# Kernel optimization log

Measured on AMD Instinct MI355X. Metric: run time of the kernel, lower is better.

Reference implementation:

```python
import jax, jax.numpy as jnp
import numpy as np

B, M, C = 32, 64, 36
INPUT_DIM, HIDDEN, N_CLASS = 1024, 512, 1000
NEG_INF = -1e10


def setup_inputs() -> dict:
    key = jax.random.key(0)
    ks = jax.random.split(key, 16)
    s = 0.02
    return {
        "mention_embeddings": jax.random.normal(ks[0], (B, M, INPUT_DIM), jnp.float32),
        "class_labels": jax.random.uniform(ks[1], (B, C, N_CLASS), jnp.float32),
        "mention_mask": jnp.ones((B, M), jnp.float32),
        "class_mask": jnp.ones((B, C), jnp.float32),
        # visual_embedder: Linear(n_class, H) -> ReLU -> Linear(H, H)
        "vw1": jax.random.normal(ks[2], (N_CLASS, HIDDEN), jnp.float32) * s,
        "vb1": jnp.zeros((HIDDEN,), jnp.float32),
        "vw2": jax.random.normal(ks[3], (HIDDEN, HIDDEN), jnp.float32) * s,
        "vb2": jnp.zeros((HIDDEN,), jnp.float32),
        # mention_embedder: Linear(input_dim, H) -> ReLU -> Linear(H, H)
        "mw1": jax.random.normal(ks[4], (INPUT_DIM, HIDDEN), jnp.float32) * s,
        "mb1": jnp.zeros((HIDDEN,), jnp.float32),
        "mw2": jax.random.normal(ks[5], (HIDDEN, HIDDEN), jnp.float32) * s,
        "mb2": jnp.zeros((HIDDEN,), jnp.float32),
        # attention: Linear(H, H) -> ReLU -> Linear(H, 1)
        "aw1": jax.random.normal(ks[6], (HIDDEN, HIDDEN), jnp.float32) * s,
        "ab1": jnp.zeros((HIDDEN,), jnp.float32),
        "aw2": jax.random.normal(ks[7], (HIDDEN, 1), jnp.float32) * s,
        "ab2": jnp.zeros((1,), jnp.float32),
    }


def reference(mention_embeddings, class_labels, mention_mask, class_mask,
              vw1, vb1, vw2, vb2, mw1, mb1, mw2, mb2, aw1, ab1, aw2, ab2):
    # visual embeddings: (B, C, H)
    vis = jax.nn.relu(class_labels @ vw1 + vb1) @ vw2 + vb2
    # mention embeddings: (B, M, H)
    men = jax.nn.relu(mention_embeddings @ mw1 + mb1) @ mw2 + mb2
    # broadcast outer product: (B, M, C, H)
    prod = men[:, :, None, :] * vis[:, None, :, :]
    # 2-layer MLP attention score -> (B, M, C)
    h = jax.nn.relu(prod @ aw1 + ab1)
    attn = (h @ aw2 + ab2)[..., 0]
    # masking
    attn = attn * mention_mask[:, :, None] * class_mask[:, None, :]
    attn = jnp.where(attn != 0, attn, NEG_INF)
    return attn
```

## Files before the change

### kernel.cpp

```cpp
#include <hip/hip_runtime.h>

typedef _Float16 f16;
typedef _Float16 f16x8 __attribute__((ext_vector_type(8)));
typedef _Float16 f16x4 __attribute__((ext_vector_type(4)));
typedef float f32x4 __attribute__((ext_vector_type(4)));
typedef float fl4 __attribute__((ext_vector_type(4)));

#define NEG_INF_F (-1e10f)

__device__ __forceinline__ void stage16(const f16* g, f16* l) {
    __builtin_amdgcn_global_load_lds((const __attribute__((address_space(1))) void*)g,
                                     (__attribute__((address_space(3))) void*)l, 16, 0, 0);
}

__global__ __launch_bounds__(256) void prep2(const float* __restrict__ me,
                                             const float* __restrict__ mw1,
                                             const float* __restrict__ vw1,
                                             const float* __restrict__ mw2,
                                             const float* __restrict__ vw2,
                                             const float* __restrict__ aw1,
                                             const float* __restrict__ cl,
                                             f16* __restrict__ me_h,
                                             f16* __restrict__ mw1t, f16* __restrict__ vw1t,
                                             f16* __restrict__ mw2t, f16* __restrict__ vw2t,
                                             f16* __restrict__ aw1t, f16* __restrict__ cl_h) {
    int bx = blockIdx.x, t = threadIdx.x;
    if (bx < 1792) {
        __shared__ float tile[32][33];
        const float* src; f16* dst; int Ksrc, Kp, tid;
        if (bx < 512)       { src = mw1; dst = mw1t; Ksrc = 1024; Kp = 1024; tid = bx; }
        else if (bx < 1024) { src = vw1; dst = vw1t; Ksrc = 1000; Kp = 1024; tid = bx - 512; }
        else if (bx < 1280) { src = mw2; dst = mw2t; Ksrc = 512;  Kp = 512;  tid = bx - 1024; }
        else if (bx < 1536) { src = vw2; dst = vw2t; Ksrc = 512;  Kp = 512;  tid = bx - 1280; }
        else                { src = aw1; dst = aw1t; Ksrc = 512;  Kp = 512;  tid = bx - 1536; }
        int tk = tid >> 4, tn = tid & 15;
        int x = t & 31, y = t >> 5;
        #pragma unroll
        for (int r = 0; r < 4; r++) {
            int k = tk * 32 + y * 4 + r;
            tile[y * 4 + r][x] = (k < Ksrc) ? src[k * 512 + tn * 32 + x] : 0.f;
        }
        __syncthreads();
        #pragma unroll
        for (int r = 0; r < 4; r++) {
            int n = tn * 32 + y * 4 + r;
            dst[n * Kp + tk * 32 + x] = (f16)tile[x][y * 4 + r];
        }
        return;
    }
    if (bx < 3840) {
        int i = (bx - 1792) * 256 + t;
        fl4 v = *(const fl4*)(me + i * 4);
        f16x4 h;
        #pragma unroll
        for (int e = 0; e < 4; e++) h[e] = (f16)v[e];
        *(f16x4*)(me_h + i * 4) = h;
        return;
    }
    {
        int i = (bx - 3840) * 256 + t;
        int idx = i * 4;
        int r = idx >> 10, k0 = idx & 1023;
        f16x4 h;
        if (k0 < 1000) {
            fl4 v = *(const fl4*)(cl + r * 1000 + k0);
            #pragma unroll
            for (int e = 0; e < 4; e++) h[e] = (f16)v[e];
        } else {
            #pragma unroll
            for (int e = 0; e < 4; e++) h[e] = (f16)0.f;
        }
        *(f16x4*)(cl_h + idx) = h;
    }
}

__global__ __launch_bounds__(256, 4) void gemm_stg3(const f16* __restrict__ Am,
                                                    const f16* __restrict__ Av,
                                                    const f16* __restrict__ Wm,
                                                    const f16* __restrict__ Wv,
                                                    const float* __restrict__ bm,
                                                    const float* __restrict__ bv,
                                                    f16* __restrict__ om,
                                                    f16* __restrict__ ov,
                                                    int K, int relu) {
    __shared__ f16 ab[4][2048], bb[4][2048];

    int t = threadIdx.x, lane = t & 63, w = t >> 6;
    int rl = lane & 15, kg = lane >> 4;
    int mq = w & 1, nq = w >> 1;
    bool isv = blockIdx.x >= 32;
    int mb = isv ? blockIdx.x - 32 : blockIdx.x;
    const f16* A = isv ? Av : Am;
    const f16* Wt = isv ? Wv : Wm;
    const float* bias = isv ? bv : bm;
    f16* out = isv ? ov : om;
    int m0 = mb * 64, n0 = blockIdx.y * 64;
    int pu = kg ^ ((rl >> 1) & 3);

    int srow = t >> 2;
    int sk8 = (t & 3) ^ ((srow >> 1) & 3);
    const f16* a_src = A + (m0 + srow) * K + sk8 * 8;
    const f16* b_src = Wt + (n0 + srow) * K + sk8 * 8;
    int ndbl = K >> 6;

    f32x4 acc[2][2] = {};

    stage16(a_src, &ab[0][t * 8]);
    stage16(b_src, &bb[0][t * 8]);
    stage16(a_src + 32, &ab[1][t * 8]);
    stage16(b_src + 32, &bb[1][t * 8]);
    __syncthreads();

    for (int ss = 0; ss < ndbl; ss++) {
        if (ss + 1 < ndbl) {
            int ka = (ss * 2 + 2) * 32, kb = (ss * 2 + 3) * 32;
            stage16(a_src + ka, &ab[(ss * 2 + 2) & 3][t * 8]);
            stage16(b_src + ka, &bb[(ss * 2 + 2) & 3][t * 8]);
            stage16(a_src + kb, &ab[(ss * 2 + 3) & 3][t * 8]);
            stage16(b_src + kb, &bb[(ss * 2 + 3) & 3][t * 8]);
        }
        #pragma unroll
        for (int h = 0; h < 2; h++) {
            int cur = (ss * 2 + h) & 3;
            f16x8 af[2], bf[2];
            #pragma unroll
            for (int f = 0; f < 2; f++) {
                af[f] = *(const f16x8*)&ab[cur][((mq * 32 + f * 16 + rl) * 4 + pu) * 8];
                bf[f] = *(const f16x8*)&bb[cur][((nq * 32 + f * 16 + rl) * 4 + pu) * 8];
            }
            #pragma unroll
            for (int fi = 0; fi < 2; fi++)
                #pragma unroll
                for (int fj = 0; fj < 2; fj++)
                    acc[fi][fj] = __builtin_amdgcn_mfma_f32_16x16x32_f16(af[fi], bf[fj], acc[fi][fj], 0, 0, 0);
        }
        __syncthreads();
    }

    #pragma unroll
    for (int fi = 0; fi < 2; fi++)
        #pragma unroll
        for (int fj = 0; fj < 2; fj++) {
            int col = n0 + nq * 32 + fj * 16 + rl;
            float bv2 = bias[col];
            #pragma unroll
            for (int r = 0; r < 4; r++) {
                int row = m0 + mq * 32 + fi * 16 + kg * 4 + r;
                float v = acc[fi][fj][r] + bv2;
                if (relu) v = fmaxf(v, 0.f);
                out[row * 512 + col] = (f16)v;
            }
        }
}

__global__ __launch_bounds__(256, 2) void attn_f14(const f16* __restrict__ men,
                                                   const f16* __restrict__ vis,
                                                   const f16* __restrict__ aw1t,
                                                   const float* __restrict__ ab1,
                                                   const float* __restrict__ aw2,
                                                   float* __restrict__ partial) {
    __shared__ f16 awb[3][4096];
    __shared__ f16 mnb[3][2048];
    __shared__ f16 vist[2048];
    __shared__ float red[2][4][64];

    int t = threadIdx.x, lane = t & 63, w = t >> 6;
    int mh = w & 1, jq = w >> 1;
    int cq = blockIdx.x, jh = blockIdx.y, b = blockIdx.z;
    int c0 = cq * 4;
    int rl = lane & 15, kg = lane >> 4;
    int pu = kg ^ ((rl >> 1) & 3);

    int srow = t >> 2;
    int sk8 = (t & 3) ^ ((srow >> 1) & 3);
    const f16* aw_src = aw1t + (jh * 128 + srow) * 512 + sk8 * 8;
    const f16* mn_src = men + (b * 64 + srow) * 512 + sk8 * 8;
    const f16* vi_src = vis + (b * 36 + c0 + (t >> 6)) * 512 + (t & 63) * 8;

    f32x4 acc[4][2][4] = {};

    stage16(vi_src, &vist[t * 8]);
    stage16(aw_src, &awb[0][t * 8]);
    stage16(aw_src + 64 * 512, &awb[0][2048 + t * 8]);
    stage16(mn_src, &mnb[0][t * 8]);
    stage16(aw_src + 32, &awb[1][t * 8]);
    stage16(aw_src + 64 * 512 + 32, &awb[1][2048 + t * 8]);
    stage16(mn_src + 32, &mnb[1][t * 8]);
    asm volatile("s_waitcnt vmcnt(3)" ::: "memory");
    __builtin_amdgcn_s_barrier();
    __builtin_amdgcn_sched_barrier(0);

    #pragma unroll
    for (int s = 0; s < 16; s++) {
        if (s > 0) {
            if (s == 15) asm volatile("s_waitcnt vmcnt(0)" ::: "memory");
            else         asm volatile("s_waitcnt vmcnt(3)" ::: "memory");
            __builtin_amdgcn_s_barrier();
            __builtin_amdgcn_sched_barrier(0);
        }
        if (s <= 13) {
            int k2 = (s + 2) * 32;
            int nb = (s + 2) % 3;
            stage16(aw_src + k2, &awb[nb][t * 8]);
            stage16(aw_src + 64 * 512 + k2, &awb[nb][2048 + t * 8]);
            stage16(mn_src + k2, &mnb[nb][t * 8]);
        }

        const int cur = s % 3;
        f16x8 mm[2], bf[4], vv[4];
        #pragma unroll
        for (int fi = 0; fi < 2; fi++)
            mm[fi] = *(const f16x8*)&mnb[cur][((mh * 32 + fi * 16 + rl) * 4 + pu) * 8];
        #pragma unroll
        for (int fj = 0; fj < 4; fj++)
            bf[fj] = *(const f16x8*)&awb[cur][((jq * 64 + fj * 16 + rl) * 4 + pu) * 8];
        #pragma unroll
        for (int c = 0; c < 4; c++)
            vv[c] = *(const f16x8*)&vist[c * 512 + s * 32 + kg * 8];

        #pragma unroll
        for (int fi = 0; fi < 2; fi++)
            #pragma unroll
            for (int c = 0; c < 4; c++) {
                f16x8 a = mm[fi] * vv[c];
                #pragma unroll
                for (int fj = 0; fj < 4; fj++)
                    acc[c][fi][fj] = __builtin_amdgcn_mfma_f32_16x16x32_f16(a, bf[fj], acc[c][fi][fj], 0, 0, 0);
            }
    }

    int j0 = jh * 128 + jq * 64;
    float ab1v[4], aw2v[4];
    #pragma unroll
    for (int fj = 0; fj < 4; fj++) {
        int j = j0 + fj * 16 + rl;
        ab1v[fj] = ab1[j];
        aw2v[fj] = aw2[j];
    }
    #pragma unroll
    for (int c = 0; c < 4; c++) {
        float part[2][4];
        #pragma unroll
        for (int fi = 0; fi < 2; fi++)
            #pragma unroll
            for (int r = 0; r < 4; r++) {
                float sv = 0.f;
                #pragma unroll
                for (int fj = 0; fj < 4; fj++)
                    sv += fmaxf(acc[c][fi][fj][r] + ab1v[fj], 0.f) * aw2v[fj];
                part[fi][r] = sv;
            }
        #pragma unroll
        for (int mask = 1; mask < 16; mask <<= 1)
            #pragma unroll
            for (int fi = 0; fi < 2; fi++)
                #pragma unroll
                for (int r = 0; r < 4; r++)
                    part[fi][r] += __shfl_xor(part[fi][r], mask);
        float myv = 0.f;
        #pragma unroll
        for (int fi = 0; fi < 2; fi++)
            #pragma unroll
            for (int r = 0; r < 4; r++)
                myv = (rl == fi * 4 + r) ? part[fi][r] : myv;
        if (rl < 8) {
            int m = mh * 32 + (rl >> 2) * 16 + kg * 4 + (rl & 3);
            red[jq][c][m] = myv;
        }
    }
    __syncthreads();

    if (t < 256) {
        int ci = t >> 6, m = t & 63;
        float s = red[0][ci][m] + red[1][ci][m];
        partial[((jh * 32 + b) * 64 + m) * 36 + c0 + ci] = s;
    }
}

__global__ __launch_bounds__(256) void postproc(const float* __restrict__ partial,
                                                const float* __restrict__ mm,
                                                const float* __restrict__ cm,
                                                const float* __restrict__ ab2,
                                                float* __restrict__ out) {
    int i = blockIdx.x * 256 + threadIdx.x;
    int b = i / 2304;
    int rest = i - b * 2304;
    int m = rest / 36, c = rest - m * 36;
    float s = 0.f;
    #pragma unroll
    for (int jh = 0; jh < 4; jh++)
        s += partial[((jh * 32 + b) * 64 + m) * 36 + c];
    float v = (s + ab2[0]) * mm[b * 64 + m] * cm[b * 36 + c];
    out[i] = (v != 0.f) ? v : NEG_INF_F;
}

extern "C" void kernel_launch(void* const* d_in, const int* in_sizes, int n_in,
                              void* d_out, int out_size, void* d_ws, size_t ws_size,
                              hipStream_t stream) {
    const float* ME  = (const float*)d_in[0];
    const float* CL  = (const float*)d_in[1];
    const float* MM  = (const float*)d_in[2];
    const float* CM  = (const float*)d_in[3];
    const float* VW1 = (const float*)d_in[4];
    const float* VB1 = (const float*)d_in[5];
    const float* VW2 = (const float*)d_in[6];
    const float* VB2 = (const float*)d_in[7];
    const float* MW1 = (const float*)d_in[8];
    const float* MB1 = (const float*)d_in[9];
    const float* MW2 = (const float*)d_in[10];
    const float* MB2 = (const float*)d_in[11];
    const float* AW1 = (const float*)d_in[12];
    const float* AB1 = (const float*)d_in[13];
    const float* AW2 = (const float*)d_in[14];
    const float* AB2 = (const float*)d_in[15];
    float* out = (float*)d_out;

    char* ws = (char*)d_ws;
    f16* me_h  = (f16*)ws; ws += (size_t)2048 * 1024 * 2;
    f16* cl_h  = (f16*)ws; ws += (size_t)1152 * 1024 * 2;
    f16* mw1t  = (f16*)ws; ws += (size_t)512 * 1024 * 2;
    f16* vw1t  = (f16*)ws; ws += (size_t)512 * 1024 * 2;
    f16* mw2t  = (f16*)ws; ws += (size_t)512 * 512 * 2;
    f16* vw2t  = (f16*)ws; ws += (size_t)512 * 512 * 2;
    f16* aw1t  = (f16*)ws; ws += (size_t)512 * 512 * 2;
    f16* men1  = (f16*)ws; ws += (size_t)2048 * 512 * 2;
    f16* menh  = (f16*)ws; ws += (size_t)2048 * 512 * 2;
    f16* vis1  = (f16*)ws; ws += (size_t)1152 * 512 * 2;
    f16* vish  = (f16*)ws; ws += (size_t)1152 * 512 * 2;
    float* part = (float*)ws; ws += (size_t)4 * 32 * 64 * 36 * 4;

    prep2<<<4992, 256, 0, stream>>>(ME, MW1, VW1, MW2, VW2, AW1, CL,
                                    me_h, mw1t, vw1t, mw2t, vw2t, aw1t, cl_h);
    gemm_stg3<<<dim3(50, 8), 256, 0, stream>>>(me_h, cl_h, mw1t, vw1t, MB1, VB1,
                                               men1, vis1, 1024, 1);
    gemm_stg3<<<dim3(50, 8), 256, 0, stream>>>(men1, vis1, mw2t, vw2t, MB2, VB2,
                                               menh, vish, 512, 0);
    attn_f14<<<dim3(9, 4, 32), 256, 0, stream>>>(menh, vish, aw1t, AB1, AW2, part);
    postproc<<<288, 256, 0, stream>>>(part, MM, CM, AB2, out);
}
```

Measured before the change: 76.02 us.

## Widen attention blocks to 512 threads covering 256 hidden columns

The attention kernel now runs 512-thread blocks, each covering 256 hidden units instead of 128, which halves the grid along the hidden dimension. The mention and visual tiles staged into shared memory are now reused by twice as many waves, cutting their redundant global loads, and postproc sums only two partials. Shared memory is unified into one 64KB buffer that is reused for the reduction, which needs an extra barrier. The trade-off is fewer blocks (576 instead of 1152) and larger per-block shared memory, which may lower occupancy.

```diff
diff --git a/kernel.cpp b/kernel.cpp
--- a/kernel.cpp
+++ b/kernel.cpp
@@ -153,67 +153,71 @@
         }
 }
 
-__global__ __launch_bounds__(256, 2) void attn_f14(const f16* __restrict__ men,
+__global__ __launch_bounds__(512, 2) void attn_f16(const f16* __restrict__ men,
                                                    const f16* __restrict__ vis,
                                                    const f16* __restrict__ aw1t,
                                                    const float* __restrict__ ab1,
                                                    const float* __restrict__ aw2,
                                                    float* __restrict__ partial) {
-    __shared__ f16 awb[3][4096];
-    __shared__ f16 mnb[3][2048];
-    __shared__ f16 vist[2048];
-    __shared__ float red[2][4][64];
+    __shared__ f16 smem[32768];
+    f16* awb  = smem;
+    f16* mnb  = smem + 24576;
+    f16* vist = smem + 30720;
+    float* red = (float*)smem;
 
     int t = threadIdx.x, lane = t & 63, w = t >> 6;
     int mh = w & 1, jq = w >> 1;
-    int cq = blockIdx.x, jh = blockIdx.y, b = blockIdx.z;
+    int cq = blockIdx.x, jh2 = blockIdx.y, b = blockIdx.z;
     int c0 = cq * 4;
     int rl = lane & 15, kg = lane >> 4;
     int pu = kg ^ ((rl >> 1) & 3);
+    bool w4 = (t < 256);
 
     int srow = t >> 2;
     int sk8 = (t & 3) ^ ((srow >> 1) & 3);
-    const f16* aw_src = aw1t + (jh * 128 + srow) * 512 + sk8 * 8;
+    const f16* aw_src = aw1t + (jh2 * 256 + srow) * 512 + sk8 * 8;
     const f16* mn_src = men + (b * 64 + srow) * 512 + sk8 * 8;
     const f16* vi_src = vis + (b * 36 + c0 + (t >> 6)) * 512 + (t & 63) * 8;
 
     f32x4 acc[4][2][4] = {};
 
-    stage16(vi_src, &vist[t * 8]);
-    stage16(aw_src, &awb[0][t * 8]);
-    stage16(aw_src + 64 * 512, &awb[0][2048 + t * 8]);
-    stage16(mn_src, &mnb[0][t * 8]);
-    stage16(aw_src + 32, &awb[1][t * 8]);
-    stage16(aw_src + 64 * 512 + 32, &awb[1][2048 + t * 8]);
-    stage16(mn_src + 32, &mnb[1][t * 8]);
-    asm volatile("s_waitcnt vmcnt(3)" ::: "memory");
+    if (w4) stage16(vi_src, &vist[t * 8]);
+    stage16(aw_src, &awb[0 * 8192 + t * 8]);
+    stage16(aw_src + 128 * 512, &awb[0 * 8192 + 4096 + t * 8]);
+    if (w4) stage16(mn_src, &mnb[0 * 2048 + t * 8]);
+    stage16(aw_src + 32, &awb[1 * 8192 + t * 8]);
+    stage16(aw_src + 128 * 512 + 32, &awb[1 * 8192 + 4096 + t * 8]);
+    if (w4) stage16(mn_src + 32, &mnb[1 * 2048 + t * 8]);
+    if (w4) asm volatile("s_waitcnt vmcnt(3)" ::: "memory");
+    else    asm volatile("s_waitcnt vmcnt(2)" ::: "memory");
     __builtin_amdgcn_s_barrier();
     __builtin_amdgcn_sched_barrier(0);
 
     #pragma unroll
     for (int s = 0; s < 16; s++) {
         if (s > 0) {
-            if (s == 15) asm volatile("s_waitcnt vmcnt(0)" ::: "memory");
-            else         asm volatile("s_waitcnt vmcnt(3)" ::: "memory");
+            if (s == 15)  asm volatile("s_waitcnt vmcnt(0)" ::: "memory");
+            else if (w4)  asm volatile("s_waitcnt vmcnt(3)" ::: "memory");
+            else          asm volatile("s_waitcnt vmcnt(2)" ::: "memory");
             __builtin_amdgcn_s_barrier();
             __builtin_amdgcn_sched_barrier(0);
         }
         if (s <= 13) {
             int k2 = (s + 2) * 32;
             int nb = (s + 2) % 3;
-            stage16(aw_src + k2, &awb[nb][t * 8]);
-            stage16(aw_src + 64 * 512 + k2, &awb[nb][2048 + t * 8]);
-            stage16(mn_src + k2, &mnb[nb][t * 8]);
+            stage16(aw_src + k2, &awb[nb * 8192 + t * 8]);
+            stage16(aw_src + 128 * 512 + k2, &awb[nb * 8192 + 4096 + t * 8]);
+            if (w4) stage16(mn_src + k2, &mnb[nb * 2048 + t * 8]);
         }
 
         const int cur = s % 3;
         f16x8 mm[2], bf[4], vv[4];
         #pragma unroll
         for (int fi = 0; fi < 2; fi++)
-            mm[fi] = *(const f16x8*)&mnb[cur][((mh * 32 + fi * 16 + rl) * 4 + pu) * 8];
+            mm[fi] = *(const f16x8*)&mnb[cur * 2048 + ((mh * 32 + fi * 16 + rl) * 4 + pu) * 8];
         #pragma unroll
         for (int fj = 0; fj < 4; fj++)
-            bf[fj] = *(const f16x8*)&awb[cur][((jq * 64 + fj * 16 + rl) * 4 + pu) * 8];
+            bf[fj] = *(const f16x8*)&awb[cur * 8192 + ((jq * 64 + fj * 16 + rl) * 4 + pu) * 8];
         #pragma unroll
         for (int c = 0; c < 4; c++)
             vv[c] = *(const f16x8*)&vist[c * 512 + s * 32 + kg * 8];
@@ -229,7 +233,7 @@
             }
     }
 
-    int j0 = jh * 128 + jq * 64;
+    int j0 = jh2 * 256 + jq * 64;
     float ab1v[4], aw2v[4];
     #pragma unroll
     for (int fj = 0; fj < 4; fj++) {
@@ -237,6 +241,7 @@
         ab1v[fj] = ab1[j];
         aw2v[fj] = aw2[j];
     }
+    __syncthreads();
     #pragma unroll
     for (int c = 0; c < 4; c++) {
         float part[2][4];
@@ -265,15 +270,16 @@
                 myv = (rl == fi * 4 + r) ? part[fi][r] : myv;
         if (rl < 8) {
             int m = mh * 32 + (rl >> 2) * 16 + kg * 4 + (rl & 3);
-            red[jq][c][m] = myv;
+            red[(jq * 4 + c) * 64 + m] = myv;
         }
     }
     __syncthreads();
 
     if (t < 256) {
         int ci = t >> 6, m = t & 63;
-        float s = red[0][ci][m] + red[1][ci][m];
-        partial[((jh * 32 + b) * 64 + m) * 36 + c0 + ci] = s;
+        float s = red[(0 * 4 + ci) * 64 + m] + red[(1 * 4 + ci) * 64 + m]
+                + red[(2 * 4 + ci) * 64 + m] + red[(3 * 4 + ci) * 64 + m];
+        partial[((jh2 * 32 + b) * 64 + m) * 36 + c0 + ci] = s;
     }
 }
 
@@ -286,10 +292,7 @@
     int b = i / 2304;
     int rest = i - b * 2304;
     int m = rest / 36, c = rest - m * 36;
-    float s = 0.f;
-    #pragma unroll
-    for (int jh = 0; jh < 4; jh++)
-        s += partial[((jh * 32 + b) * 64 + m) * 36 + c];
+    float s = partial[(b * 64 + m) * 36 + c] + partial[((32 + b) * 64 + m) * 36 + c];
     float v = (s + ab2[0]) * mm[b * 64 + m] * cm[b * 36 + c];
     out[i] = (v != 0.f) ? v : NEG_INF_F;
 }
@@ -327,7 +330,7 @@
     f16* menh  = (f16*)ws; ws += (size_t)2048 * 512 * 2;
     f16* vis1  = (f16*)ws; ws += (size_t)1152 * 512 * 2;
     f16* vish  = (f16*)ws; ws += (size_t)1152 * 512 * 2;
-    float* part = (float*)ws; ws += (size_t)4 * 32 * 64 * 36 * 4;
+    float* part = (float*)ws; ws += (size_t)2 * 32 * 64 * 36 * 4;
 
     prep2<<<4992, 256, 0, stream>>>(ME, MW1, VW1, MW2, VW2, AW1, CL,
                                     me_h, mw1t, vw1t, mw2t, vw2t, aw1t, cl_h);
@@ -335,6 +338,6 @@
                                                men1, vis1, 1024, 1);
     gemm_stg3<<<dim3(50, 8), 256, 0, stream>>>(men1, vis1, mw2t, vw2t, MB2, VB2,
                                                menh, vish, 512, 0);
-    attn_f14<<<dim3(9, 4, 32), 256, 0, stream>>>(menh, vish, aw1t, AB1, AW2, part);
+    attn_f16<<<dim3(9, 2, 32), 512, 0, stream>>>(menh, vish, aw1t, AB1, AW2, part);
     postproc<<<288, 256, 0, stream>>>(part, MM, CM, AB2, out);
 }
```

Result: slower. 82.84 us (+9.0%).
